# Kernel tuning notes

Hardware: AMD Instinct MI355X
Metric: run time of the kernel (lower is better)

The kernel has to match this reference:

```python
import jax, jax.numpy as jnp
import numpy as np

N = 50000
NEG_SLOPE = 0.2
EPS = 1e-16


def add_self_loops(edge_index, n):
    loop = jnp.arange(n, dtype=edge_index.dtype)
    src = jnp.concatenate([edge_index[0], loop])
    dst = jnp.concatenate([edge_index[1], loop])
    return src, dst


def gat_conv(x, src, dst, W, att_src, att_dst, bias, n):
    # x: [N, F_in]; W: [F_in, H*D]; att_*: [H, D]; bias: [H*D]
    H, D = att_src.shape
    h = (x @ W).reshape(n, H, D)                      # [N, H, D]
    a_src = jnp.einsum('nhd,hd->nh', h, att_src)      # [N, H]
    a_dst = jnp.einsum('nhd,hd->nh', h, att_dst)
    e = jax.nn.leaky_relu(a_src[src] + a_dst[dst], NEG_SLOPE)  # [E, H]
    # softmax over incoming edges per destination node, per head
    m = jax.ops.segment_max(e, dst, num_segments=n)   # [N, H]
    ex = jnp.exp(e - m[dst])
    s = jax.ops.segment_sum(ex, dst, num_segments=n)
    alpha = ex / (s[dst] + EPS)                       # [E, H]
    msg = h[src] * alpha[:, :, None]                  # [E, H, D]
    out = jax.ops.segment_sum(msg, dst, num_segments=n)
    return out.reshape(n, H * D) + bias


def gcn_conv(x, src, dst, W, bias, n):
    h = x @ W                                         # [N, C]
    deg = jax.ops.segment_sum(jnp.ones_like(src, dtype=h.dtype), dst, num_segments=n)
    dinv = jnp.where(deg > 0, jax.lax.rsqrt(deg), 0.0)
    norm = dinv[src] * dinv[dst]                      # [E]
    out = jax.ops.segment_sum(h[src] * norm[:, None], dst, num_segments=n)
    return out + bias


def setup_inputs() -> dict:
    key = jax.random.key(0)
    ks = jax.random.split(key, 12)
    F_in, hid, heads, ncls = 128, 32, 8, 8
    d2 = hid // 2  # 16
    E = 500000
    x = jax.random.normal(ks[0], (N, F_in), dtype=jnp.float32)
    edge_index = jax.random.randint(ks[1], (2, E), 0, N, dtype=jnp.int32)
    sc = lambda k, sh: jax.random.normal(k, sh, dtype=jnp.float32) * 0.05
    return {
        'x': x, 'edge_index': edge_index,
        'W1': sc(ks[2], (F_in, heads * hid)),
        'att_src1': sc(ks[3], (heads, hid)), 'att_dst1': sc(ks[4], (heads, hid)),
        'b1': jnp.zeros((heads * hid,), jnp.float32),
        'W2': sc(ks[5], (heads * hid, heads * d2)),
        'att_src2': sc(ks[6], (heads, d2)), 'att_dst2': sc(ks[7], (heads, d2)),
        'b2': jnp.zeros((heads * d2,), jnp.float32),
        'Wg': sc(ks[8], (heads * d2, ncls)),
        'bg': jnp.zeros((ncls,), jnp.float32),
    }


def reference(x, edge_index, W1, att_src1, att_dst1, b1, W2, att_src2, att_dst2, b2, Wg, bg):
    src, dst = add_self_loops(edge_index, N)
    h = gat_conv(x, src, dst, W1, att_src1, att_dst1, b1, N)
    h = jax.nn.relu(h)
    h = gat_conv(h, src, dst, W2, att_src2, att_dst2, b2, N)
    h = jax.nn.relu(h)
    return gcn_conv(h, src, dst, Wg, bg, N)
```

## Files before the change

kernel.cpp:

```cpp
#include <hip/hip_runtime.h>
#include <hip/hip_bf16.h>


typedef __attribute__((ext_vector_type(8))) short bf16x8;
typedef __attribute__((ext_vector_type(4))) float f32x4;


__global__ __launch_bounds__(256) void zero_deg_kernel(int* __restrict__ deg, int n) {
    int i = blockIdx.x * 256 + threadIdx.x;
    if (i < n) deg[i] = 0;
}

__global__ __launch_bounds__(256) void hist_kernel(const int* __restrict__ ei, int E, int Etot,
                                                   int* __restrict__ deg) {
    int e = blockIdx.x * 256 + threadIdx.x;
    if (e >= Etot) return;
    int d = (e < E) ? ei[E + e] : (e - E);
    atomicAdd(&deg[d], 1);
}

__global__ __launch_bounds__(256) void scanA_kernel(const int* __restrict__ deg,
                                                    int* __restrict__ off,
                                                    int* __restrict__ bsum, int n) {
    __shared__ int buf[256];
    int t = threadIdx.x;
    int i = blockIdx.x * 256 + t;
    int v = (i < n) ? deg[i] : 0;
    buf[t] = v;
    __syncthreads();
    #pragma unroll
    for (int st = 1; st < 256; st <<= 1) {
        int x = (t >= st) ? buf[t - st] : 0;
        __syncthreads();
        buf[t] += x;
        __syncthreads();
    }
    if (i < n) off[i + 1] = buf[t];
    if (t == 255) bsum[blockIdx.x] = buf[255];
}

__global__ __launch_bounds__(256) void scanB_kernel(int* __restrict__ bsum, int nb) {
    __shared__ int buf[256];
    int t = threadIdx.x;
    int v = (t < nb) ? bsum[t] : 0;
    buf[t] = v;
    __syncthreads();
    #pragma unroll
    for (int st = 1; st < 256; st <<= 1) {
        int x = (t >= st) ? buf[t - st] : 0;
        __syncthreads();
        buf[t] += x;
        __syncthreads();
    }
    if (t < nb) bsum[t] = buf[t] - v;
}

__global__ __launch_bounds__(256) void scanC_kernel(const int* __restrict__ deg,
                                                    int* __restrict__ off,
                                                    const int* __restrict__ bsum,
                                                    int* __restrict__ cur,
                                                    float* __restrict__ dinv, int n) {
    int i = blockIdx.x * 256 + threadIdx.x;
    if (i < n) {
        int o = off[i + 1] + bsum[blockIdx.x];
        off[i + 1] = o;
        cur[i] = o - deg[i];
        dinv[i] = rsqrtf((float)deg[i]);
    }
    if (i == 0) off[0] = 0;
}

__global__ __launch_bounds__(256) void scatter_kernel(const int* __restrict__ ei, int E, int Etot,
                                                      int* __restrict__ cur,
                                                      int* __restrict__ ssrc) {
    int e = blockIdx.x * 256 + threadIdx.x;
    if (e >= Etot) return;
    int s, d;
    if (e < E) { s = ei[e]; d = ei[E + e]; }
    else       { s = e - E; d = e - E; }
    int pos = atomicAdd(&cur[d], 1);
    ssrc[pos] = s;
}


__device__ __forceinline__ float4 bf4_to_f4(uint2 v) {
    float4 r;
    r.x = __uint_as_float((v.x & 0xFFFFu) << 16);
    r.y = __uint_as_float(v.x & 0xFFFF0000u);
    r.z = __uint_as_float((v.y & 0xFFFFu) << 16);
    r.w = __uint_as_float(v.y & 0xFFFF0000u);
    return r;
}

__global__ __launch_bounds__(256) void cvt_bf16_kernel(const float* __restrict__ in,
                                                       ushort* __restrict__ outb, int count) {
    int i = (blockIdx.x * 256 + threadIdx.x) * 4;
    if (i >= count) return;
    float4 v = *reinterpret_cast<const float4*>(in + i);
    ushort4 u;
    __hip_bfloat16 b0 = __float2bfloat16(v.x); u.x = *reinterpret_cast<ushort*>(&b0);
    __hip_bfloat16 b1 = __float2bfloat16(v.y); u.y = *reinterpret_cast<ushort*>(&b1);
    __hip_bfloat16 b2 = __float2bfloat16(v.z); u.z = *reinterpret_cast<ushort*>(&b2);
    __hip_bfloat16 b3 = __float2bfloat16(v.w); u.w = *reinterpret_cast<ushort*>(&b3);
    *reinterpret_cast<ushort4*>(outb + i) = u;
}

template <int K, int NC>
__global__ __launch_bounds__(256) void wtrans_kernel(const float* __restrict__ W,
                                                     ushort* __restrict__ Wt) {
    int t = blockIdx.x * 256 + threadIdx.x;
    if (t >= K * NC) return;
    int nn = t / K, k = t % K;
    __hip_bfloat16 b = __float2bfloat16(W[(size_t)k * NC + nn]);
    Wt[t] = *reinterpret_cast<ushort*>(&b);
}


template <int K, int D>
__global__ __launch_bounds__(256) void wprep_kernel(const float* __restrict__ W,
                                                    const float* __restrict__ att_s,
                                                    const float* __restrict__ att_d,
                                                    float* __restrict__ ws,
                                                    float* __restrict__ wd) {
    int t = blockIdx.x * 256 + threadIdx.x;
    if (t >= K * 8) return;
    int k = t >> 3, h = t & 7;
    const float* wrow = W + (size_t)k * (8 * D) + h * D;
    const float* as = att_s + h * D;
    const float* ad = att_d + h * D;
    float s1 = 0.f, s2 = 0.f;
    #pragma unroll
    for (int d = 0; d < D; d += 4) {
        float4 wv = *reinterpret_cast<const float4*>(wrow + d);
        float4 av = *reinterpret_cast<const float4*>(as + d);
        float4 dv = *reinterpret_cast<const float4*>(ad + d);
        s1 += wv.x * av.x + wv.y * av.y + wv.z * av.z + wv.w * av.w;
        s2 += wv.x * dv.x + wv.y * dv.y + wv.z * dv.z + wv.w * dv.w;
    }
    ws[t] = s1;
    wd[t] = s2;
}

template <int K>
__global__ __launch_bounds__(256) void adots_kernel(const ushort* __restrict__ Xb,
                                                    const float* __restrict__ ws,
                                                    const float* __restrict__ wd,
                                                    float* __restrict__ a_s,
                                                    float* __restrict__ a_d, int n) {
    int gid = blockIdx.x * 256 + threadIdx.x;
    if (gid >= n * 8) return;
    int node = gid >> 3, h = gid & 7;
    const ushort* xp = Xb + (size_t)node * K;
    float s1 = 0.f, s2 = 0.f;
    #pragma unroll 4
    for (int k = 0; k < K; k += 8) {
        uint4 v = *reinterpret_cast<const uint4*>(xp + k);
        float4 x0 = bf4_to_f4(make_uint2(v.x, v.y));
        float4 x1 = bf4_to_f4(make_uint2(v.z, v.w));
        s1 += x0.x * ws[(k + 0) * 8 + h] + x0.y * ws[(k + 1) * 8 + h] +
              x0.z * ws[(k + 2) * 8 + h] + x0.w * ws[(k + 3) * 8 + h] +
              x1.x * ws[(k + 4) * 8 + h] + x1.y * ws[(k + 5) * 8 + h] +
              x1.z * ws[(k + 6) * 8 + h] + x1.w * ws[(k + 7) * 8 + h];
        s2 += x0.x * wd[(k + 0) * 8 + h] + x0.y * wd[(k + 1) * 8 + h] +
              x0.z * wd[(k + 2) * 8 + h] + x0.w * wd[(k + 3) * 8 + h] +
              x1.x * wd[(k + 4) * 8 + h] + x1.y * wd[(k + 5) * 8 + h] +
              x1.z * wd[(k + 6) * 8 + h] + x1.w * wd[(k + 7) * 8 + h];
    }
    a_s[gid] = s1;
    a_d[gid] = s2;
}


template <int K, int NC, int BN>
__global__ __launch_bounds__(256) void mfma_gemm_kernel(const ushort* __restrict__ Ab,
                                                        const ushort* __restrict__ Bt,
                                                        ushort* __restrict__ Cb, int M) {
    constexpr int BM = 128, BK = 32;
    constexpr int FN = BN / 32;
    __shared__ ushort As[BM * BK];
    __shared__ ushort Bs[BN * BK];
    const int tid = threadIdx.x;
    const int lane = tid & 63;
    const int wid = tid >> 6;
    const int bm = blockIdx.y * BM;
    const int bn = blockIdx.x * BN;
    const int wm = (wid >> 1) * 64;
    const int wn = (wid & 1) * (BN / 2);
    const int l15 = lane & 15;
    const int l4 = lane >> 4;
    f32x4 zero4 = {0.f, 0.f, 0.f, 0.f};
    f32x4 acc[4][FN];
    #pragma unroll
    for (int i = 0; i < 4; ++i)
        #pragma unroll
        for (int j = 0; j < FN; ++j) acc[i][j] = zero4;

    for (int k0 = 0; k0 < K; k0 += BK) {
        #pragma unroll
        for (int p = 0; p < 2; ++p) {
            int ci = tid + p * 256;
            int r = ci >> 2, c = ci & 3;
            int row = bm + r;
            uint4 v = make_uint4(0, 0, 0, 0);
            if (row < M) v = *reinterpret_cast<const uint4*>(&Ab[(size_t)row * K + k0 + c * 8]);
            *reinterpret_cast<uint4*>(&As[r * BK + c * 8]) = v;
        }
        #pragma unroll
        for (int p = 0; p < BN / 64; ++p) {
            int ci = tid + p * 256;
            int r = ci >> 2, c = ci & 3;
            uint4 v = *reinterpret_cast<const uint4*>(&Bt[(size_t)(bn + r) * K + k0 + c * 8]);
            *reinterpret_cast<uint4*>(&Bs[r * BK + c * 8]) = v;
        }
        __syncthreads();
        bf16x8 af[4], bfr[FN];
        #pragma unroll
        for (int i = 0; i < 4; ++i)
            af[i] = *reinterpret_cast<const bf16x8*>(&As[(wm + 16 * i + l15) * BK + l4 * 8]);
        #pragma unroll
        for (int j = 0; j < FN; ++j)
            bfr[j] = *reinterpret_cast<const bf16x8*>(&Bs[(wn + 16 * j + l15) * BK + l4 * 8]);
        #pragma unroll
        for (int i = 0; i < 4; ++i)
            #pragma unroll
            for (int j = 0; j < FN; ++j)
                acc[i][j] = __builtin_amdgcn_mfma_f32_16x16x32_bf16(af[i], bfr[j], acc[i][j], 0, 0, 0);
        __syncthreads();
    }
    #pragma unroll
    for (int i = 0; i < 4; ++i) {
        #pragma unroll
        for (int p = 0; p < 4; ++p) {
            int row = bm + wm + 16 * i + l4 * 4 + p;
            if (row < M) {
                #pragma unroll
                for (int j = 0; j < FN; ++j) {
                    __hip_bfloat16 hb = __float2bfloat16(acc[i][j][p]);
                    Cb[(size_t)row * NC + bn + wn + 16 * j + l15] = *reinterpret_cast<ushort*>(&hb);
                }
            }
        }
    }
}


#define LRELU_EXP(e) __expf((e) > 0.f ? (e) : 0.2f * (e))

template <int C, int DH>
__global__ __launch_bounds__(256) void gat_agg_kernel(const ushort* __restrict__ hfeat,
                                                      const float* __restrict__ a_src,
                                                      const float* __restrict__ a_dst,
                                                      const int* __restrict__ off,
                                                      const int* __restrict__ ssrc,
                                                      const float* __restrict__ bias,
                                                      ushort* __restrict__ outb, int n) {
    constexpr int LR = C / 8;
    constexpr int EPS = 64 / LR;
    const int node = blockIdx.x * 4 + (threadIdx.x >> 6);
    if (node >= n) return;
    const int lane = threadIdx.x & 63;
    const int lir = lane & (LR - 1);
    const int es = lane / LR;
    const int c0 = lir * 8;
    const int h = c0 / DH;
    const float adst = a_dst[node * 8 + h];
    const int o0 = off[node], o1 = off[node + 1];
    float a0 = 0.f, a1 = 0.f, a2 = 0.f, a3 = 0.f;
    float a4 = 0.f, a5 = 0.f, a6 = 0.f, a7 = 0.f, ssum = 0.f;
    #pragma unroll 4
    for (int i = o0; i < o1; i += EPS) {
        int idx = i + es;
        bool ok = idx < o1;
        int s = ssrc[ok ? idx : (o1 - 1)];
        float e = a_src[s * 8 + h] + adst;
        float ev = ok ? LRELU_EXP(e) : 0.f;
        uint4 rv = *reinterpret_cast<const uint4*>(&hfeat[(size_t)s * C + c0]);
        float4 x0 = bf4_to_f4(make_uint2(rv.x, rv.y));
        float4 x1 = bf4_to_f4(make_uint2(rv.z, rv.w));
        ssum += ev;
        a0 += ev * x0.x; a1 += ev * x0.y; a2 += ev * x0.z; a3 += ev * x0.w;
        a4 += ev * x1.x; a5 += ev * x1.y; a6 += ev * x1.z; a7 += ev * x1.w;
    }
    #pragma unroll
    for (int m = LR; m < 64; m <<= 1) {
        ssum += __shfl_xor(ssum, m);
        a0 += __shfl_xor(a0, m); a1 += __shfl_xor(a1, m);
        a2 += __shfl_xor(a2, m); a3 += __shfl_xor(a3, m);
        a4 += __shfl_xor(a4, m); a5 += __shfl_xor(a5, m);
        a6 += __shfl_xor(a6, m); a7 += __shfl_xor(a7, m);
    }
    if (es == 0) {
        float sinv = 1.f / (ssum + 1e-16f);
        float4 bb0 = *reinterpret_cast<const float4*>(bias + c0);
        float4 bb1 = *reinterpret_cast<const float4*>(bias + c0 + 4);
        float o[8];
        o[0] = fmaxf(a0 * sinv + bb0.x, 0.f); o[1] = fmaxf(a1 * sinv + bb0.y, 0.f);
        o[2] = fmaxf(a2 * sinv + bb0.z, 0.f); o[3] = fmaxf(a3 * sinv + bb0.w, 0.f);
        o[4] = fmaxf(a4 * sinv + bb1.x, 0.f); o[5] = fmaxf(a5 * sinv + bb1.y, 0.f);
        o[6] = fmaxf(a6 * sinv + bb1.z, 0.f); o[7] = fmaxf(a7 * sinv + bb1.w, 0.f);
        ushort u[8];
        #pragma unroll
        for (int j = 0; j < 8; ++j) {
            __hip_bfloat16 hb = __float2bfloat16(o[j]);
            u[j] = *reinterpret_cast<ushort*>(&hb);
        }
        *reinterpret_cast<uint4*>(&outb[(size_t)node * C + c0]) = *reinterpret_cast<uint4*>(u);
    }
}


__global__ __launch_bounds__(256) void gcn_gemm_kernel(const ushort* __restrict__ Ab,
                                                       const float* __restrict__ Wg,
                                                       const float* __restrict__ dinv,
                                                       float* __restrict__ g, int n) {
    __shared__ float W[128 * 8];
    for (int i = threadIdx.x; i < 1024; i += 256) W[i] = Wg[i];
    __syncthreads();
    int gid = blockIdx.x * 256 + threadIdx.x;
    if (gid >= n * 8) return;
    int node = gid >> 3, c = gid & 7;
    const ushort* ap = Ab + (size_t)node * 128;
    float acc = 0.f;
    #pragma unroll
    for (int k = 0; k < 128; k += 8) {
        uint4 v = *reinterpret_cast<const uint4*>(ap + k);
        float4 x0 = bf4_to_f4(make_uint2(v.x, v.y));
        float4 x1 = bf4_to_f4(make_uint2(v.z, v.w));
        acc += x0.x * W[(k + 0) * 8 + c] + x0.y * W[(k + 1) * 8 + c] +
               x0.z * W[(k + 2) * 8 + c] + x0.w * W[(k + 3) * 8 + c] +
               x1.x * W[(k + 4) * 8 + c] + x1.y * W[(k + 5) * 8 + c] +
               x1.z * W[(k + 6) * 8 + c] + x1.w * W[(k + 7) * 8 + c];
    }
    g[gid] = acc * dinv[node];
}

__global__ __launch_bounds__(256) void gcn_agg_kernel(const float* __restrict__ g,
                                                      const float* __restrict__ dinv,
                                                      const int* __restrict__ off,
                                                      const int* __restrict__ ssrc,
                                                      const float* __restrict__ bg,
                                                      float* __restrict__ outp, int n) {
    int gid = blockIdx.x * 256 + threadIdx.x;
    if (gid >= n * 8) return;
    int node = gid >> 3, c = gid & 7;
    int o0 = off[node], o1 = off[node + 1];
    float acc = 0.f;
    for (int i = o0; i < o1; ++i) {
        int s = ssrc[i];
        acc += g[(size_t)s * 8 + c];
    }
    outp[gid] = acc * dinv[node] + bg[c];
}


extern "C" void kernel_launch(void* const* d_in, const int* in_sizes, int n_in,
                              void* d_out, int out_size, void* d_ws, size_t ws_size,
                              hipStream_t stream) {
    const float* x      = (const float*)d_in[0];
    const int*   ei     = (const int*)d_in[1];
    const float* W1     = (const float*)d_in[2];
    const float* att_s1 = (const float*)d_in[3];
    const float* att_d1 = (const float*)d_in[4];
    const float* b1     = (const float*)d_in[5];
    const float* W2     = (const float*)d_in[6];
    const float* att_s2 = (const float*)d_in[7];
    const float* att_d2 = (const float*)d_in[8];
    const float* b2     = (const float*)d_in[9];
    const float* Wg     = (const float*)d_in[10];
    const float* bg     = (const float*)d_in[11];
    float* out = (float*)d_out;

    const int n    = in_sizes[0] / 128;
    const int E    = in_sizes[1] / 2;
    const int Etot = E + n;

    float*  wsp   = (float*)d_ws;
    float*  regA  = wsp;
    float*  regB  = regA + (size_t)n * 128;
    float*  regC  = regB + (size_t)n * 128;
    float*  a_s   = regC + (size_t)n * 64;
    float*  a_d   = a_s + (size_t)n * 8;
    float*  g     = a_d + (size_t)n * 8;
    float*  dinv  = g + (size_t)n * 8;
    float*  w1s   = dinv + n;
    float*  w1d   = w1s + 1024;
    float*  w2s   = w1d + 1024;
    float*  w2d   = w2s + 2048;
    float*  w1t_f = w2d + 2048;
    float*  w2t_f = w1t_f + 16384;
    int*    off   = (int*)(w2t_f + 16384);
    int*    deg   = off + (n + 1);
    int*    cur   = deg + n;
    int*    ssrc  = cur + n;
    int*    bsum  = ssrc + Etot;

    ushort* h1b   = (ushort*)regA;
    ushort* out2b = (ushort*)regA;
    ushort* out1b = (ushort*)regB;
    ushort* xb    = (ushort*)regC;
    ushort* h2b   = (ushort*)regC;
    ushort* W1t   = (ushort*)w1t_f;
    ushort* W2t   = (ushort*)w2t_f;

    const dim3 b256(256);
    const int nch = (n + 255) / 256;

    zero_deg_kernel<<<nch, b256, 0, stream>>>(deg, n);
    hist_kernel<<<(Etot + 255) / 256, b256, 0, stream>>>(ei, E, Etot, deg);
    scanA_kernel<<<nch, b256, 0, stream>>>(deg, off, bsum, n);
    scanB_kernel<<<1, b256, 0, stream>>>(bsum, nch);
    scanC_kernel<<<nch, b256, 0, stream>>>(deg, off, bsum, cur, dinv, n);
    scatter_kernel<<<(Etot + 255) / 256, b256, 0, stream>>>(ei, E, Etot, cur, ssrc);

    wprep_kernel<128, 32><<<4, b256, 0, stream>>>(W1, att_s1, att_d1, w1s, w1d);
    wprep_kernel<256, 16><<<8, b256, 0, stream>>>(W2, att_s2, att_d2, w2s, w2d);
    cvt_bf16_kernel<<<(n * 128 / 4 + 255) / 256, b256, 0, stream>>>(x, xb, n * 128);
    wtrans_kernel<128, 256><<<(32768 + 255) / 256, b256, 0, stream>>>(W1, W1t);
    wtrans_kernel<256, 128><<<(32768 + 255) / 256, b256, 0, stream>>>(W2, W2t);

    adots_kernel<128><<<(n * 8 + 255) / 256, b256, 0, stream>>>(xb, w1s, w1d, a_s, a_d, n);
    mfma_gemm_kernel<128, 256, 128><<<dim3(2, (n + 127) / 128), b256, 0, stream>>>(xb, W1t, h1b, n);
    gat_agg_kernel<256, 32><<<(n + 3) / 4, b256, 0, stream>>>(h1b, a_s, a_d, off, ssrc, b1, out1b, n);

    adots_kernel<256><<<(n * 8 + 255) / 256, b256, 0, stream>>>(out1b, w2s, w2d, a_s, a_d, n);
    mfma_gemm_kernel<256, 128, 64><<<dim3(2, (n + 127) / 128), b256, 0, stream>>>(out1b, W2t, h2b, n);
    gat_agg_kernel<128, 16><<<(n + 3) / 4, b256, 0, stream>>>(h2b, a_s, a_d, off, ssrc, b2, out2b, n);

    gcn_gemm_kernel<<<(n * 8 + 255) / 256, b256, 0, stream>>>(out2b, Wg, dinv, g, n);
    gcn_agg_kernel<<<(n * 8 + 255) / 256, b256, 0, stream>>>(g, dinv, off, ssrc, bg, out, n);
}
```

Before: 272.5 us.

## Split GAT aggregation per head across grid and fuse prep kernels

The GAT aggregation kernel is restructured so each grid y-slice handles a single attention head. Each wave now processes edges for one head and one or more nodes, instead of one node across all heads. The edge-slot count and nodes per wave are chosen from the head dimension, which gives more parallel edge slots per head and shorter shuffle reductions. Separately, the five small preparation kernels (x bf16 convert, two weight transposes, two attention-weight folds) are merged into one launch to cut launch overhead. In exchange, the source indices and attention logits are re-read once per head, eight times in total.

```diff
diff --git a/kernel.cpp b/kernel.cpp
--- a/kernel.cpp
+++ b/kernel.cpp
@@ -92,53 +92,82 @@
     return r;
 }
 
-__global__ __launch_bounds__(256) void cvt_bf16_kernel(const float* __restrict__ in,
-                                                       ushort* __restrict__ outb, int count) {
-    int i = (blockIdx.x * 256 + threadIdx.x) * 4;
-    if (i >= count) return;
-    float4 v = *reinterpret_cast<const float4*>(in + i);
-    ushort4 u;
-    __hip_bfloat16 b0 = __float2bfloat16(v.x); u.x = *reinterpret_cast<ushort*>(&b0);
-    __hip_bfloat16 b1 = __float2bfloat16(v.y); u.y = *reinterpret_cast<ushort*>(&b1);
-    __hip_bfloat16 b2 = __float2bfloat16(v.z); u.z = *reinterpret_cast<ushort*>(&b2);
-    __hip_bfloat16 b3 = __float2bfloat16(v.w); u.w = *reinterpret_cast<ushort*>(&b3);
-    *reinterpret_cast<ushort4*>(outb + i) = u;
-}
-
-template <int K, int NC>
-__global__ __launch_bounds__(256) void wtrans_kernel(const float* __restrict__ W,
-                                                     ushort* __restrict__ Wt) {
-    int t = blockIdx.x * 256 + threadIdx.x;
-    if (t >= K * NC) return;
-    int nn = t / K, k = t % K;
-    __hip_bfloat16 b = __float2bfloat16(W[(size_t)k * NC + nn]);
-    Wt[t] = *reinterpret_cast<ushort*>(&b);
-}
-
-
-template <int K, int D>
-__global__ __launch_bounds__(256) void wprep_kernel(const float* __restrict__ W,
-                                                    const float* __restrict__ att_s,
-                                                    const float* __restrict__ att_d,
-                                                    float* __restrict__ ws,
-                                                    float* __restrict__ wd) {
-    int t = blockIdx.x * 256 + threadIdx.x;
-    if (t >= K * 8) return;
-    int k = t >> 3, h = t & 7;
-    const float* wrow = W + (size_t)k * (8 * D) + h * D;
-    const float* as = att_s + h * D;
-    const float* ad = att_d + h * D;
-    float s1 = 0.f, s2 = 0.f;
-    #pragma unroll
-    for (int d = 0; d < D; d += 4) {
-        float4 wv = *reinterpret_cast<const float4*>(wrow + d);
-        float4 av = *reinterpret_cast<const float4*>(as + d);
-        float4 dv = *reinterpret_cast<const float4*>(ad + d);
-        s1 += wv.x * av.x + wv.y * av.y + wv.z * av.z + wv.w * av.w;
-        s2 += wv.x * dv.x + wv.y * dv.y + wv.z * dv.z + wv.w * dv.w;
-    }
-    ws[t] = s1;
-    wd[t] = s2;
+__device__ __forceinline__ ushort f_to_bf(float f) {
+    __hip_bfloat16 hb = __float2bfloat16(f);
+    return *reinterpret_cast<ushort*>(&hb);
+}
+
+
+__global__ __launch_bounds__(256) void prep_kernel(const float* __restrict__ x,
+                                                   const float* __restrict__ W1,
+                                                   const float* __restrict__ W2,
+                                                   const float* __restrict__ as1,
+                                                   const float* __restrict__ ad1,
+                                                   const float* __restrict__ as2,
+                                                   const float* __restrict__ ad2,
+                                                   ushort* __restrict__ xb,
+                                                   ushort* __restrict__ W1t,
+                                                   ushort* __restrict__ W2t,
+                                                   float* __restrict__ w1s,
+                                                   float* __restrict__ w1d,
+                                                   float* __restrict__ w2s,
+                                                   float* __restrict__ w2d, int n) {
+    int gid = blockIdx.x * 256 + threadIdx.x;
+    const int NCVT = n * 32;
+    if (gid < NCVT) {
+        int i = gid * 4;
+        float4 v = *reinterpret_cast<const float4*>(x + i);
+        ushort4 u = make_ushort4(f_to_bf(v.x), f_to_bf(v.y), f_to_bf(v.z), f_to_bf(v.w));
+        *reinterpret_cast<ushort4*>(xb + i) = u;
+        return;
+    }
+    gid -= NCVT;
+    if (gid < 32768) {
+        int nn = gid >> 7, k = gid & 127;
+        W1t[gid] = f_to_bf(W1[(size_t)k * 256 + nn]);
+        return;
+    }
+    gid -= 32768;
+    if (gid < 32768) {
+        int nn = gid >> 8, k = gid & 255;
+        W2t[gid] = f_to_bf(W2[(size_t)k * 128 + nn]);
+        return;
+    }
+    gid -= 32768;
+    if (gid < 1024) {
+        int k = gid >> 3, h = gid & 7;
+        const float* wrow = W1 + (size_t)k * 256 + h * 32;
+        const float* as = as1 + h * 32;
+        const float* ad = ad1 + h * 32;
+        float s1 = 0.f, s2 = 0.f;
+        #pragma unroll
+        for (int d = 0; d < 32; d += 4) {
+            float4 wv = *reinterpret_cast<const float4*>(wrow + d);
+            float4 av = *reinterpret_cast<const float4*>(as + d);
+            float4 dv = *reinterpret_cast<const float4*>(ad + d);
+            s1 += wv.x * av.x + wv.y * av.y + wv.z * av.z + wv.w * av.w;
+            s2 += wv.x * dv.x + wv.y * dv.y + wv.z * dv.z + wv.w * dv.w;
+        }
+        w1s[gid] = s1; w1d[gid] = s2;
+        return;
+    }
+    gid -= 1024;
+    if (gid < 2048) {
+        int k = gid >> 3, h = gid & 7;
+        const float* wrow = W2 + (size_t)k * 128 + h * 16;
+        const float* as = as2 + h * 16;
+        const float* ad = ad2 + h * 16;
+        float s1 = 0.f, s2 = 0.f;
+        #pragma unroll
+        for (int d = 0; d < 16; d += 4) {
+            float4 wv = *reinterpret_cast<const float4*>(wrow + d);
+            float4 av = *reinterpret_cast<const float4*>(as + d);
+            float4 dv = *reinterpret_cast<const float4*>(ad + d);
+            s1 += wv.x * av.x + wv.y * av.y + wv.z * av.z + wv.w * av.w;
+            s2 += wv.x * dv.x + wv.y * dv.y + wv.z * dv.z + wv.w * dv.w;
+        }
+        w2s[gid] = s1; w2d[gid] = s2;
+    }
 }
 
 template <int K>
@@ -235,8 +264,7 @@
             if (row < M) {
                 #pragma unroll
                 for (int j = 0; j < FN; ++j) {
-                    __hip_bfloat16 hb = __float2bfloat16(acc[i][j][p]);
-                    Cb[(size_t)row * NC + bn + wn + 16 * j + l15] = *reinterpret_cast<ushort*>(&hb);
+                    Cb[(size_t)row * NC + bn + wn + 16 * j + l15] = f_to_bf(acc[i][j][p]);
                 }
             }
         }
@@ -247,34 +275,36 @@
 #define LRELU_EXP(e) __expf((e) > 0.f ? (e) : 0.2f * (e))
 
 template <int C, int DH>
-__global__ __launch_bounds__(256) void gat_agg_kernel(const ushort* __restrict__ hfeat,
-                                                      const float* __restrict__ a_src,
-                                                      const float* __restrict__ a_dst,
-                                                      const int* __restrict__ off,
-                                                      const int* __restrict__ ssrc,
-                                                      const float* __restrict__ bias,
-                                                      ushort* __restrict__ outb, int n) {
-    constexpr int LR = C / 8;
-    constexpr int EPS = 64 / LR;
-    const int node = blockIdx.x * 4 + (threadIdx.x >> 6);
+__global__ __launch_bounds__(256) void gat_agg_hs_kernel(const ushort* __restrict__ hfeat,
+                                                         const float* __restrict__ a_src,
+                                                         const float* __restrict__ a_dst,
+                                                         const int* __restrict__ off,
+                                                         const int* __restrict__ ssrc,
+                                                         const float* __restrict__ bias,
+                                                         ushort* __restrict__ outb, int n) {
+    constexpr int LPR = DH / 8;
+    constexpr int SLOTS = (DH == 32) ? 16 : 8;
+    constexpr int NPW = 64 / (LPR * SLOTS);
+    const int h = blockIdx.y;
+    const int lane = threadIdx.x & 63;
+    const int wave = threadIdx.x >> 6;
+    const int node = blockIdx.x * (4 * NPW) + wave * NPW + lane / (LPR * SLOTS);
     if (node >= n) return;
-    const int lane = threadIdx.x & 63;
-    const int lir = lane & (LR - 1);
-    const int es = lane / LR;
-    const int c0 = lir * 8;
-    const int h = c0 / DH;
+    const int lir = lane & (LPR - 1);
+    const int slot = (lane / LPR) & (SLOTS - 1);
+    const int coff = h * DH + lir * 8;
     const float adst = a_dst[node * 8 + h];
     const int o0 = off[node], o1 = off[node + 1];
     float a0 = 0.f, a1 = 0.f, a2 = 0.f, a3 = 0.f;
     float a4 = 0.f, a5 = 0.f, a6 = 0.f, a7 = 0.f, ssum = 0.f;
-    #pragma unroll 4
-    for (int i = o0; i < o1; i += EPS) {
-        int idx = i + es;
+    #pragma unroll 2
+    for (int i = o0; i < o1; i += SLOTS) {
+        int idx = i + slot;
         bool ok = idx < o1;
         int s = ssrc[ok ? idx : (o1 - 1)];
         float e = a_src[s * 8 + h] + adst;
         float ev = ok ? LRELU_EXP(e) : 0.f;
-        uint4 rv = *reinterpret_cast<const uint4*>(&hfeat[(size_t)s * C + c0]);
+        uint4 rv = *reinterpret_cast<const uint4*>(&hfeat[(size_t)s * C + coff]);
         float4 x0 = bf4_to_f4(make_uint2(rv.x, rv.y));
         float4 x1 = bf4_to_f4(make_uint2(rv.z, rv.w));
         ssum += ev;
@@ -282,29 +312,27 @@
         a4 += ev * x1.x; a5 += ev * x1.y; a6 += ev * x1.z; a7 += ev * x1.w;
     }
     #pragma unroll
-    for (int m = LR; m < 64; m <<= 1) {
+    for (int m = LPR; m < LPR * SLOTS; m <<= 1) {
         ssum += __shfl_xor(ssum, m);
         a0 += __shfl_xor(a0, m); a1 += __shfl_xor(a1, m);
         a2 += __shfl_xor(a2, m); a3 += __shfl_xor(a3, m);
         a4 += __shfl_xor(a4, m); a5 += __shfl_xor(a5, m);
         a6 += __shfl_xor(a6, m); a7 += __shfl_xor(a7, m);
     }
-    if (es == 0) {
+    if (slot == 0) {
         float sinv = 1.f / (ssum + 1e-16f);
-        float4 bb0 = *reinterpret_cast<const float4*>(bias + c0);
-        float4 bb1 = *reinterpret_cast<const float4*>(bias + c0 + 4);
-        float o[8];
-        o[0] = fmaxf(a0 * sinv + bb0.x, 0.f); o[1] = fmaxf(a1 * sinv + bb0.y, 0.f);
-        o[2] = fmaxf(a2 * sinv + bb0.z, 0.f); o[3] = fmaxf(a3 * sinv + bb0.w, 0.f);
-        o[4] = fmaxf(a4 * sinv + bb1.x, 0.f); o[5] = fmaxf(a5 * sinv + bb1.y, 0.f);
-        o[6] = fmaxf(a6 * sinv + bb1.z, 0.f); o[7] = fmaxf(a7 * sinv + bb1.w, 0.f);
+        float4 bb0 = *reinterpret_cast<const float4*>(bias + coff);
+        float4 bb1 = *reinterpret_cast<const float4*>(bias + coff + 4);
         ushort u[8];
-        #pragma unroll
-        for (int j = 0; j < 8; ++j) {
-            __hip_bfloat16 hb = __float2bfloat16(o[j]);
-            u[j] = *reinterpret_cast<ushort*>(&hb);
-        }
-        *reinterpret_cast<uint4*>(&outb[(size_t)node * C + c0]) = *reinterpret_cast<uint4*>(u);
+        u[0] = f_to_bf(fmaxf(a0 * sinv + bb0.x, 0.f));
+        u[1] = f_to_bf(fmaxf(a1 * sinv + bb0.y, 0.f));
+        u[2] = f_to_bf(fmaxf(a2 * sinv + bb0.z, 0.f));
+        u[3] = f_to_bf(fmaxf(a3 * sinv + bb0.w, 0.f));
+        u[4] = f_to_bf(fmaxf(a4 * sinv + bb1.x, 0.f));
+        u[5] = f_to_bf(fmaxf(a5 * sinv + bb1.y, 0.f));
+        u[6] = f_to_bf(fmaxf(a6 * sinv + bb1.z, 0.f));
+        u[7] = f_to_bf(fmaxf(a7 * sinv + bb1.w, 0.f));
+        *reinterpret_cast<uint4*>(&outb[(size_t)node * C + coff]) = *reinterpret_cast<uint4*>(u);
     }
 }
 
@@ -412,19 +440,16 @@
     scanC_kernel<<<nch, b256, 0, stream>>>(deg, off, bsum, cur, dinv, n);
     scatter_kernel<<<(Etot + 255) / 256, b256, 0, stream>>>(ei, E, Etot, cur, ssrc);
 
-    wprep_kernel<128, 32><<<4, b256, 0, stream>>>(W1, att_s1, att_d1, w1s, w1d);
-    wprep_kernel<256, 16><<<8, b256, 0, stream>>>(W2, att_s2, att_d2, w2s, w2d);
-    cvt_bf16_kernel<<<(n * 128 / 4 + 255) / 256, b256, 0, stream>>>(x, xb, n * 128);
-    wtrans_kernel<128, 256><<<(32768 + 255) / 256, b256, 0, stream>>>(W1, W1t);
-    wtrans_kernel<256, 128><<<(32768 + 255) / 256, b256, 0, stream>>>(W2, W2t);
+    prep_kernel<<<(n * 32 + 68608 + 255) / 256, b256, 0, stream>>>(
+        x, W1, W2, att_s1, att_d1, att_s2, att_d2, xb, W1t, W2t, w1s, w1d, w2s, w2d, n);
 
     adots_kernel<128><<<(n * 8 + 255) / 256, b256, 0, stream>>>(xb, w1s, w1d, a_s, a_d, n);
     mfma_gemm_kernel<128, 256, 128><<<dim3(2, (n + 127) / 128), b256, 0, stream>>>(xb, W1t, h1b, n);
-    gat_agg_kernel<256, 32><<<(n + 3) / 4, b256, 0, stream>>>(h1b, a_s, a_d, off, ssrc, b1, out1b, n);
+    gat_agg_hs_kernel<256, 32><<<dim3((n + 3) / 4, 8), b256, 0, stream>>>(h1b, a_s, a_d, off, ssrc, b1, out1b, n);
 
     adots_kernel<256><<<(n * 8 + 255) / 256, b256, 0, stream>>>(out1b, w2s, w2d, a_s, a_d, n);
     mfma_gemm_kernel<256, 128, 64><<<dim3(2, (n + 127) / 128), b256, 0, stream>>>(out1b, W2t, h2b, n);
-    gat_agg_kernel<128, 16><<<(n + 3) / 4, b256, 0, stream>>>(h2b, a_s, a_d, off, ssrc, b2, out2b, n);
+    gat_agg_hs_kernel<128, 16><<<dim3((n + 15) / 16, 8), b256, 0, stream>>>(h2b, a_s, a_d, off, ssrc, b2, out2b, n);
 
     gcn_gemm_kernel<<<(n * 8 + 255) / 256, b256, 0, stream>>>(out2b, Wg, dinv, g, n);
     gcn_agg_kernel<<<(n * 8 + 255) / 256, b256, 0, stream>>>(g, dinv, off, ssrc, bg, out, n);
```

Result: slower. 403.4 us (+48.1%).
